# Kernel optimization log

Hardware: AMD Instinct MI355X
Metric: run time of the kernel (lower is better)

## Reference

```python
import jax, jax.numpy as jnp
import numpy as np

N, E = 20000, 320000
CUR, HID, OUT, H = 256, 256, 64, 6  # cur_dim, hidden_dim, output_dim, gat heads


def setup_inputs() -> dict:
    key = jax.random.key(0)
    ks = jax.random.split(key, 16)
    p = lambda k, shape: jax.random.normal(k, shape, jnp.float32) * 0.05
    return dict(
        x=jax.random.normal(ks[0], (N, CUR), jnp.float32),
        edge_index=jax.random.randint(ks[1], (2, E), 0, N),
        edge_weight=jax.random.uniform(ks[2], (E,), jnp.float32),
        Wp=p(ks[3], (CUR, HID)), bp=p(ks[4], (HID,)),
        W_gat=p(ks[5], (HID, H * OUT)),
        att_src=p(ks[6], (H, OUT)), att_dst=p(ks[7], (H, OUT)),
        b_gat=p(ks[8], (H * OUT,)),
        W_gcn0=p(ks[9], (HID, OUT)), b_gcn0=p(ks[10], (OUT,)),
        W_gcn1=p(ks[11], (HID, OUT)), b_gcn1=p(ks[12], (OUT,)),
        W_arma_init=p(ks[13], (H * OUT, OUT)),
        W_arma_root=p(ks[14], (H * OUT, OUT)),
        b_arma=p(ks[15], (OUT,)),
    )


def _seg_sum(v, ids, n):
    return jax.ops.segment_sum(v, ids, num_segments=n)


def _gat(h, src, dst, W, a_s, a_d, b):
    # PyG GATConv: add self loops, per-edge attention, softmax over incoming edges.
    n = h.shape[0]
    loops = jnp.arange(n)
    s = jnp.concatenate([src, loops])
    d = jnp.concatenate([dst, loops])
    xw = (h @ W).reshape(n, H, OUT)               # [N,H,F]
    al = (xw * a_s).sum(-1)                       # [N,H] source term
    ar = (xw * a_d).sum(-1)                       # [N,H] target term
    e = jax.nn.leaky_relu(al[s] + ar[d], 0.2)     # [E',H]
    m = jax.ops.segment_max(e, d, num_segments=n)  # stable softmax per target
    pe = jnp.exp(e - m[d])
    alpha = pe / _seg_sum(pe, d, n)[d]
    out = _seg_sum(alpha[:, :, None] * xw[s], d, n)  # [N,H,F]
    return out.reshape(n, H * OUT) + b


def _gcn(h, src, dst, w, W, b):
    # PyG GCNConv: self loops (weight 1), symmetric D^-1/2 A D^-1/2 normalization.
    n = h.shape[0]
    loops = jnp.arange(n)
    s = jnp.concatenate([src, loops])
    d = jnp.concatenate([dst, loops])
    w2 = jnp.concatenate([w, jnp.ones((n,), h.dtype)])
    deg = _seg_sum(w2, d, n)
    dinv = jnp.where(deg > 0, jax.lax.rsqrt(deg), 0.0)
    norm = dinv[s] * w2 * dinv[d]
    xw = h @ W
    return _seg_sum(norm[:, None] * xw[s], d, n) + b


def _arma(h, src, dst, w, Wi, Wr, b):
    # PyG ARMAConv, num_stacks=1, num_layers=1, act=ReLU; gcn_norm WITHOUT self loops.
    n = h.shape[0]
    deg = _seg_sum(w, dst, n)
    dinv = jnp.where(deg > 0, jax.lax.rsqrt(deg), 0.0)
    norm = dinv[src] * w * dinv[dst]
    t = h @ Wi
    agg = _seg_sum(norm[:, None] * t[src], dst, n)
    return jax.nn.relu(agg + h @ Wr + b)


def reference(x, edge_index, edge_weight, Wp, bp, W_gat, att_src, att_dst, b_gat,
              W_gcn0, b_gcn0, W_gcn1, b_gcn1, W_arma_init, W_arma_root, b_arma):
    src, dst = edge_index[0], edge_index[1]
    h = x @ Wp + bp
    lrelu = lambda v: jax.nn.leaky_relu(v, 0.01)  # F.leaky_relu default slope
    h1 = lrelu(_gat(h, src, dst, W_gat, att_src, att_dst, b_gat))   # [N, 6*64]
    h2 = lrelu(_gcn(h, src, dst, edge_weight, W_gcn0, b_gcn0))       # [N, 64]
    h3 = lrelu(_gcn(h, src, dst, edge_weight, W_gcn1, b_gcn1))       # [N, 64]
    h4 = lrelu(_arma(h1, src, dst, edge_weight, W_arma_init, W_arma_root, b_arma))
    return jnp.tanh(jnp.concatenate([h1, h2, h3, h4], axis=1))      # [N, 576]
```

## Files before the change

kernel.cpp:

```cpp
#include <hip/hip_runtime.h>


#define NN 20000
#define EE 320000
#define GATD 384
#define NH 6
#define OUTD 64
#define ODIM 576

typedef __bf16 bf16_8 __attribute__((ext_vector_type(8)));
typedef float f32_4 __attribute__((ext_vector_type(4)));

__device__ __forceinline__ float lrelu(float x, float s) { return x > 0.f ? x : s * x; }

__device__ __forceinline__ float loadf(const void* p, size_t i, int f32) {
  return f32 ? ((const float*)p)[i] : (float)((const __bf16*)p)[i];
}

struct ProbeArgs {
  const void* ptr[15];
  int cnt[15];
  int flagidx[15];
  const int* ei;
};
__global__ void k_probe_all(ProbeArgs a, int* __restrict__ flags) {
  __shared__ int cnt;
  if (threadIdx.x == 0) cnt = 0;
  __syncthreads();
  int b = blockIdx.x;
  if (b < 15) {
    const unsigned short* u = (const unsigned short*)a.ptr[b];
    int m = a.cnt[b] < 2048 ? a.cnt[b] : 2048;
    int c = 0;
    for (int i = threadIdx.x; i < m; i += 256) {
      float v = __uint_as_float(((unsigned int)u[i]) << 16);
      if (!(fabsf(v) < 1e4f)) c++;
    }
    if (c) atomicAdd(&cnt, c);
    __syncthreads();
    if (threadIdx.x == 0) flags[a.flagidx[b]] = (cnt > m / 16) ? 1 : 0;
  } else {
    int c = 0;
    for (int i = threadIdx.x; i < 1024; i += 256)
      if (a.ei[2 * i + 1] != 0) c++;
    if (c) atomicAdd(&cnt, c);
    __syncthreads();
    if (threadIdx.x == 0) flags[16] = (cnt <= 2) ? 1 : 0;
  }
}

struct CvtSeg { const void* in; __bf16* out; int n; int flagidx; int blk0; };
struct CvtArgs { CvtSeg s[7]; };
struct TSeg { const void* in; __bf16* out; int R; int C; int flagidx; int blk0; };
struct TArgs { TSeg s[6]; };
__global__ void k_cvt_merged(CvtArgs ca, int ncvtblk, TArgs ta, const int* __restrict__ flags) {
  if ((int)blockIdx.x < ncvtblk) {
    int b = blockIdx.x;
    int k = 0;
    while (k + 1 < 7 && ca.s[k + 1].blk0 <= b) k++;
    const CvtSeg sg = ca.s[k];
    int i = (b - sg.blk0) * 256 + threadIdx.x;
    if (i >= sg.n) return;
    sg.out[i] = flags[sg.flagidx] ? (__bf16)((const float*)sg.in)[i] : ((const __bf16*)sg.in)[i];
    return;
  }
  __shared__ float t[32][33];
  int b = blockIdx.x - ncvtblk;
  int k = 0;
  while (k + 1 < 6 && ta.s[k + 1].blk0 <= b) k++;
  const TSeg sg = ta.s[k];
  int f32 = flags[sg.flagidx];
  int tpx = (sg.C + 31) >> 5;
  int lt = b - sg.blk0;
  int c0 = (lt % tpx) * 32, r0 = (lt / tpx) * 32;
  int tid = threadIdx.x;
  for (int idx = tid; idx < 1024; idx += 256) {
    int r = idx >> 5, c = idx & 31;
    if (r0 + r < sg.R && c0 + c < sg.C)
      t[r][c] = loadf(sg.in, (size_t)(r0 + r) * sg.C + (c0 + c), f32);
  }
  __syncthreads();
  for (int idx = tid; idx < 1024; idx += 256) {
    int r = idx >> 5, c = idx & 31;
    if (c0 + r < sg.C && r0 + c < sg.R)
      sg.out[(size_t)(c0 + r) * sg.R + (r0 + c)] = (__bf16)t[c][r];
  }
}

__global__ void k_count(const int* __restrict__ ei, const void* __restrict__ ew,
                        const int* __restrict__ flags,
                        int* __restrict__ deg, float* __restrict__ wdeg) {
  int e = blockIdx.x * 256 + threadIdx.x;
  if (e >= EE) return;
  int sh = flags[16];
  int d = ei[(size_t)(EE + e) << sh];
  atomicAdd(&deg[d], 1);
  atomicAdd(&wdeg[d], loadf(ew, e, flags[2]));
}

__global__ __launch_bounds__(256) void k_scan1(const int* __restrict__ deg,
                                               int* __restrict__ bsum) {
  int i = blockIdx.x * 256 + threadIdx.x;
  int v = (i < NN) ? deg[i] : 0;
  for (int off = 32; off; off >>= 1) v += __shfl_xor(v, off);
  __shared__ int ws[4];
  if ((threadIdx.x & 63) == 0) ws[threadIdx.x >> 6] = v;
  __syncthreads();
  if (threadIdx.x == 0) bsum[blockIdx.x] = ws[0] + ws[1] + ws[2] + ws[3];
}

__global__ __launch_bounds__(256) void k_scan2(const int* __restrict__ deg,
    const int* __restrict__ bsum, const float* __restrict__ wdeg,
    int* __restrict__ rowstart, float* __restrict__ dg, float* __restrict__ da) {
  int b = blockIdx.x;
  int tid = threadIdx.x;
  int lane = tid & 63, wv = tid >> 6;
  int i = b * 256 + tid;
  __shared__ int red[4];
  __shared__ int wsum2[4];
  __shared__ int sbase;
  {
    int v = (tid < b) ? bsum[tid] : 0;
    for (int off = 32; off; off >>= 1) v += __shfl_xor(v, off);
    if (lane == 0) red[wv] = v;
    __syncthreads();
    if (tid == 0) sbase = red[0] + red[1] + red[2] + red[3];
    __syncthreads();
  }
  int v = (i < NN) ? deg[i] : 0;
  int run = v;
  for (int off = 1; off < 64; off <<= 1) {
    int u = __shfl_up(run, off);
    if (lane >= off) run += u;
  }
  if (lane == 63) wsum2[wv] = run;
  __syncthreads();
  int wb = 0;
#pragma unroll
  for (int w = 0; w < 4; w++) { int x = wsum2[w]; if (w < wv) wb += x; }
  int excl = sbase + wb + run - v;
  if (i < NN) rowstart[i] = excl;
  if (i == NN - 1) rowstart[NN] = excl + v;
  if (i < NN) {
    float w = wdeg[i];
    dg[i] = rsqrtf(w + 1.0f);
    da[i] = w > 0.f ? rsqrtf(w) : 0.f;
  }
}

__global__ void k_fill(const int* __restrict__ ei, const void* __restrict__ ew,
                       const int* __restrict__ flags, const int* __restrict__ rowstart,
                       int* __restrict__ cursor,
                       int* __restrict__ csr_src, float* __restrict__ csr_w) {
  int e = blockIdx.x * 256 + threadIdx.x;
  if (e >= EE) return;
  int sh = flags[16];
  int d = ei[(size_t)(EE + e) << sh];
  int s = ei[(size_t)e << sh];
  int pos = rowstart[d] + atomicAdd(&cursor[d], 1);
  csr_src[pos] = s;
  csr_w[pos] = loadf(ew, e, flags[2]);
}

template<bool HAS_BIAS>
__global__ __launch_bounds__(256) void gemm64(const void* __restrict__ A,
    const int* __restrict__ aflag, const __bf16* __restrict__ Bt,
    const __bf16* __restrict__ bias,
    __bf16* __restrict__ C1, int n1, int ldc1,
    __bf16* __restrict__ C2, int ldc2,
    int M, int K) {
  __shared__ __bf16 Al[64][40];
  __shared__ __bf16 Bl[128][40];
  int a32 = *aflag;
  int tid = threadIdx.x;
  int w = tid >> 6, lane = tid & 63;
  int quad = lane >> 4, r = lane & 15;
  int row0 = blockIdx.x * 64, col0 = blockIdx.y * 128;
  f32_4 acc[4][2] = {};
  int srow = tid >> 2;
  int koff = (tid & 3) * 8;
  int brow = tid >> 1;
  int bko  = (tid & 1) * 16;
  for (int kt = 0; kt < K; kt += 32) {
    int arow = row0 + srow;
    if (a32) {
      float4 a0 = {0.f, 0.f, 0.f, 0.f}, a1 = {0.f, 0.f, 0.f, 0.f};
      if (arow < M) {
        const float* ap = (const float*)A + (size_t)arow * K + kt + koff;
        a0 = *(const float4*)ap;
        a1 = *(const float4*)(ap + 4);
      }
      bf16_8 t;
      t[0] = (__bf16)a0.x; t[1] = (__bf16)a0.y; t[2] = (__bf16)a0.z; t[3] = (__bf16)a0.w;
      t[4] = (__bf16)a1.x; t[5] = (__bf16)a1.y; t[6] = (__bf16)a1.z; t[7] = (__bf16)a1.w;
      *(bf16_8*)(&Al[srow][koff]) = t;
    } else {
      float4 av = {0.f, 0.f, 0.f, 0.f};
      if (arow < M) av = *(const float4*)((const __bf16*)A + (size_t)arow * K + kt + koff);
      *(float4*)(&Al[srow][koff]) = av;
    }
    const __bf16* bp = Bt + (size_t)(col0 + brow) * K + kt + bko;
    *(float4*)(&Bl[brow][bko])     = *(const float4*)bp;
    *(float4*)(&Bl[brow][bko + 8]) = *(const float4*)(bp + 8);
    __syncthreads();
    bf16_8 bfrag0 = *(const bf16_8*)(&Bl[w * 16 + r][quad * 8]);
    bf16_8 bfrag1 = *(const bf16_8*)(&Bl[64 + w * 16 + r][quad * 8]);
#pragma unroll
    for (int mt = 0; mt < 4; mt++) {
      bf16_8 afrag = *(const bf16_8*)(&Al[mt * 16 + r][quad * 8]);
      acc[mt][0] = __builtin_amdgcn_mfma_f32_16x16x32_bf16(afrag, bfrag0, acc[mt][0], 0, 0, 0);
      acc[mt][1] = __builtin_amdgcn_mfma_f32_16x16x32_bf16(afrag, bfrag1, acc[mt][1], 0, 0, 0);
    }
    __syncthreads();
  }
  __bf16* Cp; int ldc; int cbase;
  if (col0 < n1) { Cp = C1; ldc = ldc1; cbase = col0; }
  else           { Cp = C2; ldc = ldc2; cbase = col0 - n1; }
  int cc0 = cbase + w * 16 + r;
  int cc1 = cbase + 64 + w * 16 + r;
  float bv0 = HAS_BIAS ? (float)bias[col0 + w * 16 + r] : 0.0f;
  float bv1 = HAS_BIAS ? (float)bias[col0 + 64 + w * 16 + r] : 0.0f;
#pragma unroll
  for (int mt = 0; mt < 4; mt++) {
#pragma unroll
    for (int rr = 0; rr < 4; rr++) {
      int crow = row0 + mt * 16 + quad * 4 + rr;
      if (crow < M) {
        Cp[(size_t)crow * ldc + cc0] = (__bf16)(acc[mt][0][rr] + bv0);
        Cp[(size_t)crow * ldc + cc1] = (__bf16)(acc[mt][1][rr] + bv1);
      }
    }
  }
}

__global__ void k_alar_w(const __bf16* __restrict__ xwb, const __bf16* __restrict__ as_,
                         const __bf16* __restrict__ ad_,
                         float* __restrict__ al, float* __restrict__ ar) {
  int p = blockIdx.x * 4 + (threadIdx.x >> 6);
  int lane = threadIdx.x & 63;
  if (p >= NN * NH) return;
  int i = p / NH, h = p - i * NH;
  float xv = (float)xwb[(size_t)i * GATD + h * OUTD + lane];
  float s1 = xv * (float)as_[h * OUTD + lane];
  float s2 = xv * (float)ad_[h * OUTD + lane];
  for (int off = 32; off; off >>= 1) { s1 += __shfl_xor(s1, off); s2 += __shfl_xor(s2, off); }
  if (lane == 0) { al[p] = s1; ar[p] = s2; }
}

__global__ __launch_bounds__(256) void k_gat2(const __bf16* __restrict__ xwb,
    const float* __restrict__ al, const float* __restrict__ ar,
    const int* __restrict__ rowstart, const int* __restrict__ csr_src,
    const __bf16* __restrict__ bgat,
    __bf16* __restrict__ h1b, float* __restrict__ out) {
  int wv = threadIdx.x >> 6, lane = threadIdx.x & 63;
  int i = blockIdx.x * 4 + wv;
  __shared__ int   src_sh[4][64];
  __shared__ float ex_sh[4][64][NH];
  __shared__ int   mc_sh[4];
  int e0 = rowstart[i], e1 = rowstart[i + 1];
  if (lane == 0) mc_sh[wv] = (e1 - e0 + 63) >> 6;
  float arv[NH], exs[NH], acc[NH], denp[NH];
#pragma unroll
  for (int h = 0; h < NH; h++) arv[h] = ar[i * NH + h];
#pragma unroll
  for (int h = 0; h < NH; h++) {
    float e = lrelu(al[i * NH + h] + arv[h], 0.2f);
    exs[h] = __expf(e);
    acc[h] = exs[h] * (float)xwb[(size_t)i * GATD + h * OUTD + lane];
    denp[h] = 0.f;
  }
  __syncthreads();
  int mch = max(max(mc_sh[0], mc_sh[1]), max(mc_sh[2], mc_sh[3]));
  for (int c = 0; c < mch; c++) {
    if (c) __syncthreads();
    int base = e0 + c * 64;
    int cnt = e1 - base; cnt = cnt < 0 ? 0 : (cnt > 64 ? 64 : cnt);
    if (lane < cnt) {
      int s = csr_src[base + lane];
      src_sh[wv][lane] = s;
#pragma unroll
      for (int h = 0; h < NH; h++) {
        float ex = __expf(lrelu(al[s * NH + h] + arv[h], 0.2f));
        ex_sh[wv][lane][h] = ex;
        denp[h] += ex;
      }
    }
    __syncthreads();
    int j = 0;
    for (; j + 2 <= cnt; j += 2) {
      int s0 = src_sh[wv][j], s1 = src_sh[wv][j + 1];
      const __bf16* r0 = xwb + (size_t)s0 * GATD + lane;
      const __bf16* r1 = xwb + (size_t)s1 * GATD + lane;
      float x0[NH], x1[NH];
#pragma unroll
      for (int h = 0; h < NH; h++) { x0[h] = (float)r0[h * OUTD]; x1[h] = (float)r1[h * OUTD]; }
#pragma unroll
      for (int h = 0; h < NH; h++)
        acc[h] += ex_sh[wv][j][h] * x0[h] + ex_sh[wv][j + 1][h] * x1[h];
    }
    if (j < cnt) {
      int s0 = src_sh[wv][j];
      const __bf16* r0 = xwb + (size_t)s0 * GATD + lane;
#pragma unroll
      for (int h = 0; h < NH; h++) acc[h] += ex_sh[wv][j][h] * (float)r0[h * OUTD];
    }
  }
#pragma unroll
  for (int h = 0; h < NH; h++) {
    float d = denp[h];
    for (int off = 32; off; off >>= 1) d += __shfl_xor(d, off);
    d += exs[h];
    float v = acc[h] / d + (float)bgat[h * OUTD + lane];
    v = lrelu(v, 0.01f);
    h1b[(size_t)i * GATD + h * OUTD + lane] = (__bf16)v;
    out[(size_t)i * ODIM + h * OUTD + lane] = tanhf(v);
  }
}

__global__ __launch_bounds__(256) void k_gcnarma2(const __bf16* __restrict__ xwgb,
    const __bf16* __restrict__ trb, const int* __restrict__ rowstart,
    const int* __restrict__ csr_src, const float* __restrict__ csr_w,
    const float* __restrict__ dgcn, const float* __restrict__ darma,
    const __bf16* __restrict__ b0, const __bf16* __restrict__ b1,
    const __bf16* __restrict__ ba, float* __restrict__ out) {
  int wv = threadIdx.x >> 6, lane = threadIdx.x & 63;
  int i = blockIdx.x * 4 + wv;
  __shared__ int   src_sh[4][64];
  __shared__ float wg_sh[4][64], wa_sh[4][64];
  __shared__ int   mc_sh[4];
  int e0 = rowstart[i], e1 = rowstart[i + 1];
  if (lane == 0) mc_sh[wv] = (e1 - e0 + 63) >> 6;
  __syncthreads();
  int mch = max(max(mc_sh[0], mc_sh[1]), max(mc_sh[2], mc_sh[3]));
  float g0 = 0.f, g1 = 0.f, aa = 0.f;
  for (int c = 0; c < mch; c++) {
    if (c) __syncthreads();
    int base = e0 + c * 64;
    int cnt = e1 - base; cnt = cnt < 0 ? 0 : (cnt > 64 ? 64 : cnt);
    if (lane < cnt) {
      int eidx = base + lane;
      int s = csr_src[eidx];
      float wvv = csr_w[eidx];
      src_sh[wv][lane] = s;
      wg_sh[wv][lane] = dgcn[s] * wvv;
      wa_sh[wv][lane] = darma[s] * wvv;
    }
    __syncthreads();
    int j = 0;
    for (; j + 2 <= cnt; j += 2) {
      int s0 = src_sh[wv][j], s1 = src_sh[wv][j + 1];
      float wg0 = wg_sh[wv][j], wg1 = wg_sh[wv][j + 1];
      float wa0 = wa_sh[wv][j], wa1 = wa_sh[wv][j + 1];
      const __bf16* p0 = xwgb + (size_t)s0 * 128;
      const __bf16* p1 = xwgb + (size_t)s1 * 128;
      const __bf16* q0 = trb + (size_t)s0 * 128;
      const __bf16* q1 = trb + (size_t)s1 * 128;
      g0 += wg0 * (float)p0[lane] + wg1 * (float)p1[lane];
      g1 += wg0 * (float)p0[lane + 64] + wg1 * (float)p1[lane + 64];
      aa += wa0 * (float)q0[lane] + wa1 * (float)q1[lane];
    }
    if (j < cnt) {
      int s0 = src_sh[wv][j];
      float wg0 = wg_sh[wv][j], wa0 = wa_sh[wv][j];
      const __bf16* p0 = xwgb + (size_t)s0 * 128;
      const __bf16* q0 = trb + (size_t)s0 * 128;
      g0 += wg0 * (float)p0[lane];
      g1 += wg0 * (float)p0[lane + 64];
      aa += wa0 * (float)q0[lane];
    }
  }
  float di = dgcn[i];
  float v0 = lrelu(di * g0 + di * di * (float)xwgb[(size_t)i * 128 + lane] + (float)b0[lane], 0.01f);
  float v1 = lrelu(di * g1 + di * di * (float)xwgb[(size_t)i * 128 + 64 + lane] + (float)b1[lane], 0.01f);
  out[(size_t)i * ODIM + 384 + lane] = tanhf(v0);
  out[(size_t)i * ODIM + 448 + lane] = tanhf(v1);
  float va = darma[i] * aa + (float)trb[(size_t)i * 128 + 64 + lane] + (float)ba[lane];
  va = fmaxf(va, 0.f);
  out[(size_t)i * ODIM + 512 + lane] = tanhf(va);
}

extern "C" void kernel_launch(void* const* d_in, const int* in_sizes, int n_in,
                              void* d_out, int out_size, void* d_ws, size_t ws_size,
                              hipStream_t stream) {
  const int* ei = (const int*)d_in[1];
  float* out = (float*)d_out;

  char* ws = (char*)d_ws;
  size_t off = 0;
  auto alloc = [&](size_t bytes) -> void* {
    void* p = ws + off;
    off += (bytes + 255) & ~(size_t)255;
    return p;
  };
  int*    flags    = (int*)alloc(32 * 4);
  int*    deg      = (int*)alloc((size_t)3 * NN * 4);
  int*    cursor   = deg + NN;
  float*  wdeg     = (float*)(deg + 2 * NN);
  int*    bsum     = (int*)alloc(128 * 4);
  int*    rowstart = (int*)alloc((size_t)(NN + 1) * 4);
  int*    csr_src  = (int*)alloc((size_t)EE * 4);
  float*  csr_w    = (float*)alloc((size_t)EE * 4);
  float*  dgcn     = (float*)alloc((size_t)NN * 4);
  float*  darma    = (float*)alloc((size_t)NN * 4);
  float*  al       = (float*)alloc((size_t)NN * NH * 4);
  float*  ar       = (float*)alloc((size_t)NN * NH * 4);
  __bf16* bpb   = (__bf16*)alloc(256 * 2);
  __bf16* asb   = (__bf16*)alloc(384 * 2);
  __bf16* adb   = (__bf16*)alloc(384 * 2);
  __bf16* bgatb = (__bf16*)alloc(384 * 2);
  __bf16* bg0b  = (__bf16*)alloc(64 * 2);
  __bf16* bg1b  = (__bf16*)alloc(64 * 2);
  __bf16* bab   = (__bf16*)alloc(64 * 2);
  __bf16* Wp_t    = (__bf16*)alloc(256 * 256 * 2);
  __bf16* Wcat_t  = (__bf16*)alloc((size_t)(384 + 128) * 256 * 2);
  __bf16* Wgat_t  = Wcat_t;
  __bf16* Wg01_t  = Wcat_t + (size_t)384 * 256;
  __bf16* Warma_t = (__bf16*)alloc(128 * 384 * 2);
  char* regA = (char*)alloc((size_t)NN * GATD * 2);
  __bf16* h   = (__bf16*)regA;
  __bf16* h1b = (__bf16*)regA;
  char* regB = (char*)alloc((size_t)NN * GATD * 2);
  __bf16* xwb = (__bf16*)regB;
  __bf16* trb = (__bf16*)regB;
  __bf16* xwgb = (__bf16*)alloc((size_t)NN * 128 * 2);
  (void)ws_size; (void)in_sizes; (void)n_in; (void)out_size;

  hipMemsetAsync(ws, 0, 256 + (size_t)3 * NN * 4, stream);

  dim3 tb(256);
  ProbeArgs pa;
  const int pidx[15] = {0, 2, 3, 4, 5, 6, 7, 8, 9, 10, 11, 12, 13, 14, 15};
  const int pcnt[15] = {NN * 256, EE, 256 * 256, 256, 256 * 384, NH * OUTD, NH * OUTD,
                        NH * OUTD, 256 * 64, 64, 256 * 64, 64, GATD * OUTD, GATD * OUTD, 64};
  for (int k = 0; k < 15; k++) { pa.ptr[k] = d_in[pidx[k]]; pa.cnt[k] = pcnt[k]; pa.flagidx[k] = pidx[k]; }
  pa.ei = ei;
  k_probe_all<<<dim3(16), tb, 0, stream>>>(pa, flags);

  CvtArgs ca;
  TArgs ta;
  int cvtblk = 0, tblk = 0;
  {
    struct { int idx; __bf16* out; int n; } cv[7] = {
      {4, bpb, 256}, {6, asb, 384}, {7, adb, 384}, {8, bgatb, 384},
      {10, bg0b, 64}, {12, bg1b, 64}, {15, bab, 64},
    };
    for (int k = 0; k < 7; k++) {
      ca.s[k].in = d_in[cv[k].idx]; ca.s[k].out = cv[k].out; ca.s[k].n = cv[k].n;
      ca.s[k].flagidx = cv[k].idx; ca.s[k].blk0 = cvtblk;
      cvtblk += (cv[k].n + 255) / 256;
    }
    struct { int idx; __bf16* out; int R; int C; } tv[6] = {
      {3,  Wp_t,             256, 256},
      {5,  Wgat_t,           256, 384},
      {9,  Wg01_t,           256, 64},
      {11, Wg01_t + 64 * 256, 256, 64},
      {13, Warma_t,          384, 64},
      {14, Warma_t + 64 * 384, 384, 64},
    };
    for (int k = 0; k < 6; k++) {
      ta.s[k].in = d_in[tv[k].idx]; ta.s[k].out = tv[k].out;
      ta.s[k].R = tv[k].R; ta.s[k].C = tv[k].C;
      ta.s[k].flagidx = tv[k].idx; ta.s[k].blk0 = tblk;
      tblk += ((tv[k].R + 31) / 32) * ((tv[k].C + 31) / 32);
    }
    k_cvt_merged<<<dim3(cvtblk + tblk), tb, 0, stream>>>(ca, cvtblk, ta, flags);
  }

  const int NBLK = (NN + 255) / 256;
  k_count<<<dim3((EE + 255) / 256), tb, 0, stream>>>(ei, d_in[2], flags, deg, wdeg);
  k_scan1<<<dim3(NBLK), tb, 0, stream>>>(deg, bsum);
  k_scan2<<<dim3(NBLK), tb, 0, stream>>>(deg, bsum, wdeg, rowstart, dgcn, darma);
  k_fill<<<dim3((EE + 255) / 256), tb, 0, stream>>>(ei, d_in[2], flags, rowstart, cursor, csr_src, csr_w);

  const int MB64 = (NN + 63) / 64;
  gemm64<true ><<<dim3(MB64, 2), tb, 0, stream>>>(d_in[0], &flags[0], Wp_t, bpb,
                                                  h, 256, 256, nullptr, 0, NN, 256);
  gemm64<false><<<dim3(MB64, 4), tb, 0, stream>>>(h, &flags[30], Wcat_t, nullptr,
                                                  xwb, 384, 384, xwgb, 128, NN, 256);
  k_alar_w<<<dim3((NN * NH + 3) / 4), tb, 0, stream>>>(xwb, asb, adb, al, ar);
  k_gat2<<<dim3(NN / 4), tb, 0, stream>>>(xwb, al, ar, rowstart, csr_src, bgatb, h1b, out);
  gemm64<false><<<dim3(MB64, 1), tb, 0, stream>>>(h1b, &flags[30], Warma_t, nullptr,
                                                  trb, 128, 128, nullptr, 0, NN, 384);
  k_gcnarma2<<<dim3(NN / 4), tb, 0, stream>>>(xwgb, trb, rowstart, csr_src, csr_w,
                                              dgcn, darma, bg0b, bg1b, bab, out);
}
```

Measured before the change: 296.2 us.

## Fuse GCN aggregation into GAT edge pass and batch ARMA gathers

Moves the two GCN neighbor aggregations into the GAT aggregation kernel so they share one CSR traversal, source-index load and edge-loop overhead. The ARMA aggregation becomes its own lighter kernel. That kernel pads each edge chunk to a multiple of 8 (padded entries point at the node itself with zero weight), reads indices and weights with vector LDS loads, and issues 8 independent gathers per step for more memory-level parallelism. In exchange the GAT kernel needs more registers and does more work per edge, which may lower occupancy. The padding also adds a few wasted gathers per node.

After: 295.8 us. Within noise of the previous version (-0.1%).

```diff
diff --git a/kernel.cpp b/kernel.cpp
--- a/kernel.cpp
+++ b/kernel.cpp
@@ -247,15 +247,19 @@
   if (lane == 0) { al[p] = s1; ar[p] = s2; }
 }
 
-__global__ __launch_bounds__(256) void k_gat2(const __bf16* __restrict__ xwb,
+__global__ __launch_bounds__(256) void k_gatgcn(const __bf16* __restrict__ xwb,
+    const __bf16* __restrict__ xwgb,
     const float* __restrict__ al, const float* __restrict__ ar,
     const int* __restrict__ rowstart, const int* __restrict__ csr_src,
-    const __bf16* __restrict__ bgat,
+    const float* __restrict__ csr_w, const float* __restrict__ dgcn,
+    const __bf16* __restrict__ bgat, const __bf16* __restrict__ b0,
+    const __bf16* __restrict__ b1,
     __bf16* __restrict__ h1b, float* __restrict__ out) {
   int wv = threadIdx.x >> 6, lane = threadIdx.x & 63;
   int i = blockIdx.x * 4 + wv;
   __shared__ int   src_sh[4][64];
   __shared__ float ex_sh[4][64][NH];
+  __shared__ float wg_sh[4][64];
   __shared__ int   mc_sh[4];
   int e0 = rowstart[i], e1 = rowstart[i + 1];
   if (lane == 0) mc_sh[wv] = (e1 - e0 + 63) >> 6;
@@ -269,6 +273,7 @@
     acc[h] = exs[h] * (float)xwb[(size_t)i * GATD + h * OUTD + lane];
     denp[h] = 0.f;
   }
+  float g0 = 0.f, g1 = 0.f;
   __syncthreads();
   int mch = max(max(mc_sh[0], mc_sh[1]), max(mc_sh[2], mc_sh[3]));
   for (int c = 0; c < mch; c++) {
@@ -276,8 +281,10 @@
     int base = e0 + c * 64;
     int cnt = e1 - base; cnt = cnt < 0 ? 0 : (cnt > 64 ? 64 : cnt);
     if (lane < cnt) {
-      int s = csr_src[base + lane];
+      int eidx = base + lane;
+      int s = csr_src[eidx];
       src_sh[wv][lane] = s;
+      wg_sh[wv][lane] = dgcn[s] * csr_w[eidx];
 #pragma unroll
       for (int h = 0; h < NH; h++) {
         float ex = __expf(lrelu(al[s * NH + h] + arv[h], 0.2f));
@@ -291,18 +298,29 @@
       int s0 = src_sh[wv][j], s1 = src_sh[wv][j + 1];
       const __bf16* r0 = xwb + (size_t)s0 * GATD + lane;
       const __bf16* r1 = xwb + (size_t)s1 * GATD + lane;
+      const __bf16* p0 = xwgb + (size_t)s0 * 128;
+      const __bf16* p1 = xwgb + (size_t)s1 * 128;
       float x0[NH], x1[NH];
 #pragma unroll
       for (int h = 0; h < NH; h++) { x0[h] = (float)r0[h * OUTD]; x1[h] = (float)r1[h * OUTD]; }
+      float y00 = (float)p0[lane], y01 = (float)p0[lane + 64];
+      float y10 = (float)p1[lane], y11 = (float)p1[lane + 64];
+      float wg0 = wg_sh[wv][j], wg1 = wg_sh[wv][j + 1];
 #pragma unroll
       for (int h = 0; h < NH; h++)
         acc[h] += ex_sh[wv][j][h] * x0[h] + ex_sh[wv][j + 1][h] * x1[h];
+      g0 += wg0 * y00 + wg1 * y10;
+      g1 += wg0 * y01 + wg1 * y11;
     }
     if (j < cnt) {
       int s0 = src_sh[wv][j];
       const __bf16* r0 = xwb + (size_t)s0 * GATD + lane;
+      const __bf16* p0 = xwgb + (size_t)s0 * 128;
+      float wg0 = wg_sh[wv][j];
 #pragma unroll
       for (int h = 0; h < NH; h++) acc[h] += ex_sh[wv][j][h] * (float)r0[h * OUTD];
+      g0 += wg0 * (float)p0[lane];
+      g1 += wg0 * (float)p0[lane + 64];
     }
   }
 #pragma unroll
@@ -315,65 +333,56 @@
     h1b[(size_t)i * GATD + h * OUTD + lane] = (__bf16)v;
     out[(size_t)i * ODIM + h * OUTD + lane] = tanhf(v);
   }
-}
-
-__global__ __launch_bounds__(256) void k_gcnarma2(const __bf16* __restrict__ xwgb,
-    const __bf16* __restrict__ trb, const int* __restrict__ rowstart,
-    const int* __restrict__ csr_src, const float* __restrict__ csr_w,
-    const float* __restrict__ dgcn, const float* __restrict__ darma,
-    const __bf16* __restrict__ b0, const __bf16* __restrict__ b1,
-    const __bf16* __restrict__ ba, float* __restrict__ out) {
-  int wv = threadIdx.x >> 6, lane = threadIdx.x & 63;
-  int i = blockIdx.x * 4 + wv;
-  __shared__ int   src_sh[4][64];
-  __shared__ float wg_sh[4][64], wa_sh[4][64];
-  __shared__ int   mc_sh[4];
-  int e0 = rowstart[i], e1 = rowstart[i + 1];
-  if (lane == 0) mc_sh[wv] = (e1 - e0 + 63) >> 6;
-  __syncthreads();
-  int mch = max(max(mc_sh[0], mc_sh[1]), max(mc_sh[2], mc_sh[3]));
-  float g0 = 0.f, g1 = 0.f, aa = 0.f;
-  for (int c = 0; c < mch; c++) {
-    if (c) __syncthreads();
-    int base = e0 + c * 64;
-    int cnt = e1 - base; cnt = cnt < 0 ? 0 : (cnt > 64 ? 64 : cnt);
-    if (lane < cnt) {
-      int eidx = base + lane;
-      int s = csr_src[eidx];
-      float wvv = csr_w[eidx];
-      src_sh[wv][lane] = s;
-      wg_sh[wv][lane] = dgcn[s] * wvv;
-      wa_sh[wv][lane] = darma[s] * wvv;
-    }
-    __syncthreads();
-    int j = 0;
-    for (; j + 2 <= cnt; j += 2) {
-      int s0 = src_sh[wv][j], s1 = src_sh[wv][j + 1];
-      float wg0 = wg_sh[wv][j], wg1 = wg_sh[wv][j + 1];
-      float wa0 = wa_sh[wv][j], wa1 = wa_sh[wv][j + 1];
-      const __bf16* p0 = xwgb + (size_t)s0 * 128;
-      const __bf16* p1 = xwgb + (size_t)s1 * 128;
-      const __bf16* q0 = trb + (size_t)s0 * 128;
-      const __bf16* q1 = trb + (size_t)s1 * 128;
-      g0 += wg0 * (float)p0[lane] + wg1 * (float)p1[lane];
-      g1 += wg0 * (float)p0[lane + 64] + wg1 * (float)p1[lane + 64];
-      aa += wa0 * (float)q0[lane] + wa1 * (float)q1[lane];
-    }
-    if (j < cnt) {
-      int s0 = src_sh[wv][j];
-      float wg0 = wg_sh[wv][j], wa0 = wa_sh[wv][j];
-      const __bf16* p0 = xwgb + (size_t)s0 * 128;
-      const __bf16* q0 = trb + (size_t)s0 * 128;
-      g0 += wg0 * (float)p0[lane];
-      g1 += wg0 * (float)p0[lane + 64];
-      aa += wa0 * (float)q0[lane];
-    }
-  }
   float di = dgcn[i];
   float v0 = lrelu(di * g0 + di * di * (float)xwgb[(size_t)i * 128 + lane] + (float)b0[lane], 0.01f);
   float v1 = lrelu(di * g1 + di * di * (float)xwgb[(size_t)i * 128 + 64 + lane] + (float)b1[lane], 0.01f);
   out[(size_t)i * ODIM + 384 + lane] = tanhf(v0);
   out[(size_t)i * ODIM + 448 + lane] = tanhf(v1);
+}
+
+__global__ __launch_bounds__(256) void k_arma(const __bf16* __restrict__ trb,
+    const int* __restrict__ rowstart, const int* __restrict__ csr_src,
+    const float* __restrict__ csr_w, const float* __restrict__ darma,
+    const __bf16* __restrict__ ba, float* __restrict__ out) {
+  int wv = threadIdx.x >> 6, lane = threadIdx.x & 63;
+  int i = blockIdx.x * 4 + wv;
+  __shared__ __attribute__((aligned(16))) int   src_sh[4][64];
+  __shared__ __attribute__((aligned(16))) float wa_sh[4][64];
+  __shared__ int mc_sh[4];
+  int e0 = rowstart[i], e1 = rowstart[i + 1];
+  if (lane == 0) mc_sh[wv] = (e1 - e0 + 63) >> 6;
+  __syncthreads();
+  int mch = max(max(mc_sh[0], mc_sh[1]), max(mc_sh[2], mc_sh[3]));
+  float aa = 0.f;
+  for (int c = 0; c < mch; c++) {
+    if (c) __syncthreads();
+    int base = e0 + c * 64;
+    int cnt = e1 - base; cnt = cnt < 0 ? 0 : (cnt > 64 ? 64 : cnt);
+    int s = i; float wav = 0.f;
+    if (lane < cnt) {
+      int eidx = base + lane;
+      s = csr_src[eidx];
+      wav = darma[s] * csr_w[eidx];
+    }
+    src_sh[wv][lane] = s;
+    wa_sh[wv][lane] = wav;
+    __syncthreads();
+    int cntp = (cnt + 7) & ~7;
+    for (int j = 0; j < cntp; j += 8) {
+      int4 sa = *(const int4*)&src_sh[wv][j];
+      int4 sb = *(const int4*)&src_sh[wv][j + 4];
+      int sq[8] = {sa.x, sa.y, sa.z, sa.w, sb.x, sb.y, sb.z, sb.w};
+      float tq[8];
+#pragma unroll
+      for (int q = 0; q < 8; q++)
+        tq[q] = (float)trb[(size_t)sq[q] * 128 + lane];
+      float4 wa0 = *(const float4*)&wa_sh[wv][j];
+      float4 wa1 = *(const float4*)&wa_sh[wv][j + 4];
+      float waq[8] = {wa0.x, wa0.y, wa0.z, wa0.w, wa1.x, wa1.y, wa1.z, wa1.w};
+#pragma unroll
+      for (int q = 0; q < 8; q++) aa += waq[q] * tq[q];
+    }
+  }
   float va = darma[i] * aa + (float)trb[(size_t)i * 128 + 64 + lane] + (float)ba[lane];
   va = fmaxf(va, 0.f);
   out[(size_t)i * ODIM + 512 + lane] = tanhf(va);
@@ -478,9 +487,10 @@
   gemm64<false><<<dim3(MB64, 4), tb, 0, stream>>>(h, &flags[30], Wcat_t, nullptr,
                                                   xwb, 384, 384, xwgb, 128, NN, 256);
   k_alar_w<<<dim3((NN * NH + 3) / 4), tb, 0, stream>>>(xwb, asb, adb, al, ar);
-  k_gat2<<<dim3(NN / 4), tb, 0, stream>>>(xwb, al, ar, rowstart, csr_src, bgatb, h1b, out);
+  k_gatgcn<<<dim3(NN / 4), tb, 0, stream>>>(xwb, xwgb, al, ar, rowstart, csr_src,
+                                            csr_w, dgcn, bgatb, bg0b, bg1b, h1b, out);
   gemm64<false><<<dim3(MB64, 1), tb, 0, stream>>>(h1b, &flags[30], Warma_t, nullptr,
                                                   trb, 128, 128, nullptr, 0, NN, 384);
-  k_gcnarma2<<<dim3(NN / 4), tb, 0, stream>>>(xwgb, trb, rowstart, csr_src, csr_w,
-                                              dgcn, darma, bg0b, bg1b, bab, out);
-}
+  k_arma<<<dim3(NN / 4), tb, 0, stream>>>(trb, rowstart, csr_src, csr_w,
+                                          darma, bab, out);
+}
```
